# Kernel tuning notes

Hardware: AMD Instinct MI355X
Metric: run time of the kernel (lower is better)

## Reference

```python
import jax, jax.numpy as jnp
import numpy as np

E = 500_000
D = 128
A = 16
HID = 128
G = 25_000
IN = 2 * D + A  # 272


def setup_inputs() -> dict:
    key = jax.random.key(0)
    ks = jax.random.split(key, 8)
    src_emb = jax.random.normal(ks[0], (E, D), dtype=jnp.float32)
    dst_emb = jax.random.normal(ks[1], (E, D), dtype=jnp.float32)
    edge_attr = jax.random.normal(ks[2], (E, A), dtype=jnp.float32)
    group_index = jax.random.randint(ks[3], (E,), 0, G, dtype=jnp.int64)
    # MLP params: LazyLinear(IN->HID), Linear(HID->1)
    W1 = jax.random.normal(ks[4], (IN, HID), dtype=jnp.float32) * (1.0 / np.sqrt(IN))
    b1 = jnp.zeros((HID,), dtype=jnp.float32)
    W2 = jax.random.normal(ks[5], (HID, 1), dtype=jnp.float32) * (1.0 / np.sqrt(HID))
    b2 = jnp.zeros((1,), dtype=jnp.float32)
    return {
        "src_emb": src_emb,
        "dst_emb": dst_emb,
        "edge_attr": edge_attr,
        "W1": W1,
        "b1": b1,
        "W2": W2,
        "b2": b2,
        "group_index": group_index,
        "num_groups": G,
    }


def reference(src_emb, dst_emb, edge_attr, W1, b1, W2, b2, group_index, num_groups):
    # features: [E, 2D+A]
    features = jnp.concatenate([src_emb, dst_emb, edge_attr], axis=-1)
    h = jax.nn.relu(features @ W1 + b1)            # [E, HID]
    logits = (h @ W2 + b2)[:, 0]                   # [E]
    # single-pass segment softmax (replaces per-group python loop)
    lf = logits.astype(jnp.float32)
    seg_max = jax.ops.segment_max(lf, group_index, num_segments=num_groups)  # [G]
    # empty segments give -inf max; edges never index them, so safe
    ex = jnp.exp(lf - seg_max[group_index])        # [E]
    seg_sum = jax.ops.segment_sum(ex, group_index, num_segments=num_groups)  # [G]
    weights = (ex / seg_sum[group_index]).astype(logits.dtype)[:, None]      # [E, 1]
    return weights, logits
```

## Files before the change

### kernel.cpp

```cpp
#include <hip/hip_runtime.h>
#include <stdint.h>

#define E_N   500000
#define G_N   25000
#define HIDN  128
#define KIN   272
#define KPAD  288
#define NKSTEP 9

typedef short bfrag_t __attribute__((ext_vector_type(8)));
typedef float accf4  __attribute__((ext_vector_type(4)));

__device__ __forceinline__ uint32_t pack2_bf16(float a, float b) {
    uint32_t ua = __builtin_bit_cast(uint32_t, a);
    uint32_t ub = __builtin_bit_cast(uint32_t, b);
    ua += 0x7FFFu + ((ua >> 16) & 1u);
    ub += 0x7FFFu + ((ub >> 16) & 1u);
    return (ua >> 16) | (ub & 0xFFFF0000u);
}

__global__ void prep_kernel(const float* __restrict__ W1, float* __restrict__ seg_sum,
                            ushort* __restrict__ Wb) {
    int t = blockIdx.x * 256 + threadIdx.x;
    if (t < G_N) seg_sum[t] = 0.0f;
    if (t < HIDN * KPAD) {
        int n = t / KPAD;
        int k = t - n * KPAD;
        ushort v = 0;
        if (k < KIN) {
            uint32_t u = __builtin_bit_cast(uint32_t, W1[k * HIDN + n]);
            u += 0x7FFFu + ((u >> 16) & 1u);
            v = (ushort)(u >> 16);
        }
        Wb[t] = v;
    }
}

__launch_bounds__(256, 2)
__global__ void mlp_kernel(const float* __restrict__ src, const float* __restrict__ dst,
                           const float* __restrict__ attr, const ushort* __restrict__ Wb,
                           const float* __restrict__ b1, const float* __restrict__ W2,
                           const float* __restrict__ b2, const int* __restrict__ gidx,
                           float* __restrict__ logits_out, float* __restrict__ ex_out,
                           float* __restrict__ seg_sum) {
    __shared__ __align__(16) ushort Alds[256 * 32];
    __shared__ __align__(16) ushort Blds[128 * 32];

    const int tid  = threadIdx.x;
    const int lane = tid & 63;
    const int wave = tid >> 6;
    const int blk_row = blockIdx.x * 256;

    accf4 acc[4][8];
    #pragma unroll
    for (int a = 0; a < 4; ++a)
        #pragma unroll
        for (int b = 0; b < 8; ++b)
            acc[a][b] = (accf4)(0.0f);

    const int rsub = tid >> 3;
    const int col4 = tid & 7;

    for (int s = 0; s < NKSTEP; ++s) {
        __syncthreads();

        const float* bp; int rstride; bool vcol;
        if (s < 4)      { bp = src  + s * 32 + col4 * 4;        rstride = 128; vcol = true; }
        else if (s < 8) { bp = dst  + (s - 4) * 32 + col4 * 4;  rstride = 128; vcol = true; }
        else            { bp = attr + col4 * 4;                 rstride = 16;  vcol = (col4 < 4); }

        #pragma unroll
        for (int j = 0; j < 8; ++j) {
            int rl = j * 32 + rsub;
            int grow = blk_row + rl;
            float4 v = {0.f, 0.f, 0.f, 0.f};
            if (vcol && grow < E_N) v = *(const float4*)(bp + (size_t)grow * rstride);
            uint2 p;
            p.x = pack2_bf16(v.x, v.y);
            p.y = pack2_bf16(v.z, v.w);
            *(uint2*)&Alds[rl * 32 + col4 * 4] = p;
        }

        #pragma unroll
        for (int i = 0; i < 2; ++i) {
            int c  = i * 256 + tid;
            int n  = c >> 2;
            int ko = (c & 3) * 8;
            uint4 w = *(const uint4*)(Wb + n * KPAD + s * 32 + ko);
            *(uint4*)&Blds[c * 8] = w;
        }

        __syncthreads();

        bfrag_t afrag[4];
        #pragma unroll
        for (int a = 0; a < 4; ++a)
            afrag[a] = *(const bfrag_t*)&Alds[(wave * 64 + a * 16 + (lane & 15)) * 32 + (lane >> 4) * 8];
        #pragma unroll
        for (int b = 0; b < 8; ++b) {
            bfrag_t bfrag = *(const bfrag_t*)&Blds[(b * 16 + (lane & 15)) * 32 + (lane >> 4) * 8];
            #pragma unroll
            for (int a = 0; a < 4; ++a)
                acc[a][b] = __builtin_amdgcn_mfma_f32_16x16x32_bf16(afrag[a], bfrag, acc[a][b], 0, 0, 0);
        }
    }

    const int cbase = lane & 15;
    const int quad  = lane >> 4;
    float w2v[8], b1v[8];
    #pragma unroll
    for (int b = 0; b < 8; ++b) {
        w2v[b] = W2[b * 16 + cbase];
        b1v[b] = b1[b * 16 + cbase];
    }
    const float bias2 = b2[0];

    #pragma unroll
    for (int a = 0; a < 4; ++a) {
        float p[4] = {0.f, 0.f, 0.f, 0.f};
        #pragma unroll
        for (int b = 0; b < 8; ++b) {
            #pragma unroll
            for (int r = 0; r < 4; ++r) {
                float h = acc[a][b][r] + b1v[b];
                h = h > 0.f ? h : 0.f;
                p[r] += h * w2v[b];
            }
        }
        #pragma unroll
        for (int r = 0; r < 4; ++r) {
            float v = p[r];
            v += __shfl_xor(v, 1);
            v += __shfl_xor(v, 2);
            v += __shfl_xor(v, 4);
            v += __shfl_xor(v, 8);
            if (cbase == 0) {
                int grow = blk_row + wave * 64 + a * 16 + quad * 4 + r;
                if (grow < E_N) {
                    float logit = v + bias2;
                    logits_out[grow] = logit;
                    float ex = __expf(logit);
                    ex_out[grow] = ex;
                    atomicAdd(&seg_sum[gidx[grow]], ex);
                }
            }
        }
    }
}

__global__ void norm_kernel(const float* __restrict__ ex, const float* __restrict__ seg_sum,
                            const int* __restrict__ gidx, float* __restrict__ wout) {
    int e = blockIdx.x * 256 + threadIdx.x;
    if (e < E_N) wout[e] = ex[e] / seg_sum[gidx[e]];
}

extern "C" void kernel_launch(void* const* d_in, const int* in_sizes, int n_in,
                              void* d_out, int out_size, void* d_ws, size_t ws_size,
                              hipStream_t stream) {
    const float* src  = (const float*)d_in[0];
    const float* dst  = (const float*)d_in[1];
    const float* attr = (const float*)d_in[2];
    const float* W1   = (const float*)d_in[3];
    const float* b1   = (const float*)d_in[4];
    const float* W2   = (const float*)d_in[5];
    const float* b2   = (const float*)d_in[6];
    const int*   gidx = (const int*)d_in[7];

    float* weights_out = (float*)d_out;
    float* logits_out  = (float*)d_out + E_N;

    char* ws = (char*)d_ws;
    ushort* Wb  = (ushort*)ws;
    float*  seg = (float*)(ws + 73728);
    float*  ex  = (float*)(ws + 73728 + 100000);

    prep_kernel<<<(HIDN * KPAD + 255) / 256, 256, 0, stream>>>(W1, seg, Wb);

    const int nblk = (E_N + 255) / 256;
    mlp_kernel<<<nblk, 256, 0, stream>>>(src, dst, attr, Wb, b1, W2, b2, gidx,
                                         logits_out, ex, seg);
    norm_kernel<<<nblk, 256, 0, stream>>>(ex, seg, gidx, weights_out);
}
```

Measured before the change: 628.8 us.

## Drop LDS staging; load MFMA fragments directly from global with pre-swizzled weights

The prep kernel now writes W1 as bf16 already laid out in per-lane MFMA fragment order. The MLP kernel then loads both A and B fragments straight from global memory into registers, so the shared-memory staging and per-step __syncthreads are gone. Each block now covers 128 rows instead of 256, with 32 rows per wave, and launch bounds are raised to 3 blocks per CU to reach more occupancy. The cost is that every wave re-reads the weight fragments from global memory or L2, and input loads become 32-byte per-lane reads rather than coalesced block-wide loads.

```diff
diff --git a/kernel.cpp b/kernel.cpp
--- a/kernel.cpp
+++ b/kernel.cpp
@@ -5,7 +5,6 @@
 #define G_N   25000
 #define HIDN  128
 #define KIN   272
-#define KPAD  288
 #define NKSTEP 9
 
 typedef short bfrag_t __attribute__((ext_vector_type(8)));
@@ -23,119 +22,113 @@
                             ushort* __restrict__ Wb) {
     int t = blockIdx.x * 256 + threadIdx.x;
     if (t < G_N) seg_sum[t] = 0.0f;
-    if (t < HIDN * KPAD) {
-        int n = t / KPAD;
-        int k = t - n * KPAD;
-        ushort v = 0;
-        if (k < KIN) {
-            uint32_t u = __builtin_bit_cast(uint32_t, W1[k * HIDN + n]);
-            u += 0x7FFFu + ((u >> 16) & 1u);
-            v = (ushort)(u >> 16);
-        }
-        Wb[t] = v;
+    int j    = t & 7;
+    int lane = (t >> 3) & 63;
+    int sb   = t >> 9;
+    int b    = sb & 7;
+    int s    = sb >> 3;
+    int k    = s * 32 + (lane >> 4) * 8 + j;
+    int n    = b * 16 + (lane & 15);
+    ushort v = 0;
+    if (k < KIN) {
+        uint32_t u = __builtin_bit_cast(uint32_t, W1[k * HIDN + n]);
+        u += 0x7FFFu + ((u >> 16) & 1u);
+        v = (ushort)(u >> 16);
     }
+    Wb[t] = v;
 }
 
-__launch_bounds__(256, 2)
+__launch_bounds__(256, 3)
 __global__ void mlp_kernel(const float* __restrict__ src, const float* __restrict__ dst,
                            const float* __restrict__ attr, const ushort* __restrict__ Wb,
                            const float* __restrict__ b1, const float* __restrict__ W2,
                            const float* __restrict__ b2, const int* __restrict__ gidx,
                            float* __restrict__ logits_out, float* __restrict__ ex_out,
                            float* __restrict__ seg_sum) {
-    __shared__ __align__(16) ushort Alds[256 * 32];
-    __shared__ __align__(16) ushort Blds[128 * 32];
-
     const int tid  = threadIdx.x;
     const int lane = tid & 63;
     const int wave = tid >> 6;
-    const int blk_row = blockIdx.x * 256;
+    const int m    = lane & 15;
+    const int q    = lane >> 4;
+    const int rowbase = blockIdx.x * 128 + wave * 32;
 
-    accf4 acc[4][8];
+    const int  r0 = rowbase + m,  r1 = rowbase + 16 + m;
+    const bool v0 = r0 < E_N,     v1 = r1 < E_N;
+
+    accf4 acc[2][8];
     #pragma unroll
-    for (int a = 0; a < 4; ++a)
+    for (int a = 0; a < 2; ++a)
         #pragma unroll
         for (int b = 0; b < 8; ++b)
             acc[a][b] = (accf4)(0.0f);
 
-    const int rsub = tid >> 3;
-    const int col4 = tid & 7;
+    #pragma unroll
+    for (int s = 0; s < NKSTEP; ++s) {
+        bfrag_t bf[8];
+        #pragma unroll
+        for (int b = 0; b < 8; ++b)
+            bf[b] = *(const bfrag_t*)(Wb + (size_t)((s * 8 + b) * 64 + lane) * 8);
 
-    for (int s = 0; s < NKSTEP; ++s) {
-        __syncthreads();
-
-        const float* bp; int rstride; bool vcol;
-        if (s < 4)      { bp = src  + s * 32 + col4 * 4;        rstride = 128; vcol = true; }
-        else if (s < 8) { bp = dst  + (s - 4) * 32 + col4 * 4;  rstride = 128; vcol = true; }
-        else            { bp = attr + col4 * 4;                 rstride = 16;  vcol = (col4 < 4); }
-
+        bfrag_t af[2];
         #pragma unroll
-        for (int j = 0; j < 8; ++j) {
-            int rl = j * 32 + rsub;
-            int grow = blk_row + rl;
-            float4 v = {0.f, 0.f, 0.f, 0.f};
-            if (vcol && grow < E_N) v = *(const float4*)(bp + (size_t)grow * rstride);
-            uint2 p;
-            p.x = pack2_bf16(v.x, v.y);
-            p.y = pack2_bf16(v.z, v.w);
-            *(uint2*)&Alds[rl * 32 + col4 * 4] = p;
+        for (int a = 0; a < 2; ++a) {
+            const int  rr = a ? r1 : r0;
+            const bool vv = a ? v1 : v0;
+            float4 x0 = {0.f, 0.f, 0.f, 0.f}, x1 = {0.f, 0.f, 0.f, 0.f};
+            if (s < 8) {
+                const float* base  = (s < 4) ? src : dst;
+                const int coloff   = (s < 4) ? s * 32 : (s - 4) * 32;
+                const float* p = base + (size_t)rr * 128 + coloff + q * 8;
+                if (vv) { x0 = ((const float4*)p)[0]; x1 = ((const float4*)p)[1]; }
+            } else {
+                if (vv && q < 2) {
+                    const float* p = attr + (size_t)rr * 16 + q * 8;
+                    x0 = ((const float4*)p)[0]; x1 = ((const float4*)p)[1];
+                }
+            }
+            uint4 u;
+            u.x = pack2_bf16(x0.x, x0.y);
+            u.y = pack2_bf16(x0.z, x0.w);
+            u.z = pack2_bf16(x1.x, x1.y);
+            u.w = pack2_bf16(x1.z, x1.w);
+            af[a] = *(bfrag_t*)&u;
         }
 
         #pragma unroll
-        for (int i = 0; i < 2; ++i) {
-            int c  = i * 256 + tid;
-            int n  = c >> 2;
-            int ko = (c & 3) * 8;
-            uint4 w = *(const uint4*)(Wb + n * KPAD + s * 32 + ko);
-            *(uint4*)&Blds[c * 8] = w;
-        }
-
-        __syncthreads();
-
-        bfrag_t afrag[4];
-        #pragma unroll
-        for (int a = 0; a < 4; ++a)
-            afrag[a] = *(const bfrag_t*)&Alds[(wave * 64 + a * 16 + (lane & 15)) * 32 + (lane >> 4) * 8];
-        #pragma unroll
-        for (int b = 0; b < 8; ++b) {
-            bfrag_t bfrag = *(const bfrag_t*)&Blds[(b * 16 + (lane & 15)) * 32 + (lane >> 4) * 8];
+        for (int b = 0; b < 8; ++b)
             #pragma unroll
-            for (int a = 0; a < 4; ++a)
-                acc[a][b] = __builtin_amdgcn_mfma_f32_16x16x32_bf16(afrag[a], bfrag, acc[a][b], 0, 0, 0);
-        }
+            for (int a = 0; a < 2; ++a)
+                acc[a][b] = __builtin_amdgcn_mfma_f32_16x16x32_bf16(af[a], bf[b], acc[a][b], 0, 0, 0);
     }
 
-    const int cbase = lane & 15;
-    const int quad  = lane >> 4;
     float w2v[8], b1v[8];
     #pragma unroll
     for (int b = 0; b < 8; ++b) {
-        w2v[b] = W2[b * 16 + cbase];
-        b1v[b] = b1[b * 16 + cbase];
+        w2v[b] = W2[b * 16 + m];
+        b1v[b] = b1[b * 16 + m];
     }
     const float bias2 = b2[0];
 
     #pragma unroll
-    for (int a = 0; a < 4; ++a) {
-        float p[4] = {0.f, 0.f, 0.f, 0.f};
+    for (int a = 0; a < 2; ++a) {
+        float p4[4] = {0.f, 0.f, 0.f, 0.f};
         #pragma unroll
-        for (int b = 0; b < 8; ++b) {
+        for (int b = 0; b < 8; ++b)
             #pragma unroll
-            for (int r = 0; r < 4; ++r) {
-                float h = acc[a][b][r] + b1v[b];
+            for (int rr = 0; rr < 4; ++rr) {
+                float h = acc[a][b][rr] + b1v[b];
                 h = h > 0.f ? h : 0.f;
-                p[r] += h * w2v[b];
+                p4[rr] += h * w2v[b];
             }
-        }
         #pragma unroll
-        for (int r = 0; r < 4; ++r) {
-            float v = p[r];
+        for (int rr = 0; rr < 4; ++rr) {
+            float v = p4[rr];
             v += __shfl_xor(v, 1);
             v += __shfl_xor(v, 2);
             v += __shfl_xor(v, 4);
             v += __shfl_xor(v, 8);
-            if (cbase == 0) {
-                int grow = blk_row + wave * 64 + a * 16 + quad * 4 + r;
+            if (m == 0) {
+                int grow = rowbase + a * 16 + q * 4 + rr;
                 if (grow < E_N) {
                     float logit = v + bias2;
                     logits_out[grow] = logit;
@@ -172,12 +165,12 @@
     char* ws = (char*)d_ws;
     ushort* Wb  = (ushort*)ws;
     float*  seg = (float*)(ws + 73728);
-    float*  ex  = (float*)(ws + 73728 + 100000);
+    float*  ex  = (float*)(ws + 173728);
 
-    prep_kernel<<<(HIDN * KPAD + 255) / 256, 256, 0, stream>>>(W1, seg, Wb);
+    prep_kernel<<<144, 256, 0, stream>>>(W1, seg, Wb);
 
-    const int nblk = (E_N + 255) / 256;
+    const int nblk = (E_N + 127) / 128;
     mlp_kernel<<<nblk, 256, 0, stream>>>(src, dst, attr, Wb, b1, W2, b2, gidx,
                                          logits_out, ex, seg);
-    norm_kernel<<<nblk, 256, 0, stream>>>(ex, seg, gidx, weights_out);
+    norm_kernel<<<(E_N + 255) / 256, 256, 0, stream>>>(ex, seg, gidx, weights_out);
 }
```

Result: faster. 550.9 us (-12.4%).
